# Kernel optimization log

Measured on AMD Instinct MI355X. Metric: run time of the kernel, lower is better.

Reference implementation:

```python
import jax, jax.numpy as jnp
import numpy as np

N_NODES = 16384
N_EDGES = 131072
EDGE_DIM = 16
IN_CH = 32
OUT_CH = 32
HID_EDGE = 64
MLP_HID = 64  # int(32 * 2.0)
OUT_FINAL = 10
N_GRAPHS = 64
BN_EPS = 1e-5


def setup_inputs() -> dict:
    key = jax.random.key(0)
    ks = jax.random.split(key, 20)
    s = lambda *sh: 1.0 / np.sqrt(sh[0])
    inp = {
        'x': jax.random.normal(ks[0], (N_NODES, IN_CH), jnp.float32),
        'edge_attr': jax.random.normal(ks[1], (N_EDGES, EDGE_DIM), jnp.float32),
        'edge_index': jax.random.randint(ks[2], (2, N_EDGES), 0, N_NODES, jnp.int64),
        'batch': jnp.sort(jax.random.randint(ks[3], (N_NODES,), 0, N_GRAPHS, jnp.int64)),
    }
    # layer 0: edge MLP (EDGE_DIM->HID_EDGE->IN_CH*OUT_CH), root, bias, BN affine
    inp['w1_0'] = jax.random.normal(ks[4], (EDGE_DIM, HID_EDGE), jnp.float32) * s(EDGE_DIM)
    inp['b1_0'] = jnp.zeros((HID_EDGE,), jnp.float32)
    inp['w2_0'] = jax.random.normal(ks[5], (HID_EDGE, IN_CH * OUT_CH), jnp.float32) * s(HID_EDGE)
    inp['b2_0'] = jnp.zeros((IN_CH * OUT_CH,), jnp.float32)
    inp['root_0'] = jax.random.normal(ks[6], (IN_CH, OUT_CH), jnp.float32) * s(IN_CH)
    inp['bias_0'] = jnp.zeros((OUT_CH,), jnp.float32)
    inp['gamma_0'] = jnp.ones((OUT_CH,), jnp.float32)
    inp['beta_0'] = jnp.zeros((OUT_CH,), jnp.float32)
    # layer 1: edge MLP (EDGE_DIM->HID_EDGE->OUT_CH*OUT_CH)
    inp['w1_1'] = jax.random.normal(ks[7], (EDGE_DIM, HID_EDGE), jnp.float32) * s(EDGE_DIM)
    inp['b1_1'] = jnp.zeros((HID_EDGE,), jnp.float32)
    inp['w2_1'] = jax.random.normal(ks[8], (HID_EDGE, OUT_CH * OUT_CH), jnp.float32) * s(HID_EDGE)
    inp['b2_1'] = jnp.zeros((OUT_CH * OUT_CH,), jnp.float32)
    inp['root_1'] = jax.random.normal(ks[9], (OUT_CH, OUT_CH), jnp.float32) * s(OUT_CH)
    inp['bias_1'] = jnp.zeros((OUT_CH,), jnp.float32)
    inp['gamma_1'] = jnp.ones((OUT_CH,), jnp.float32)
    inp['beta_1'] = jnp.zeros((OUT_CH,), jnp.float32)
    # final MLP (dropout is identity in eval / deterministic reference)
    inp['mlp_w1'] = jax.random.normal(ks[10], (OUT_CH, MLP_HID), jnp.float32) * s(OUT_CH)
    inp['mlp_b1'] = jnp.zeros((MLP_HID,), jnp.float32)
    inp['mlp_w2'] = jax.random.normal(ks[11], (MLP_HID, OUT_FINAL), jnp.float32) * s(MLP_HID)
    inp['mlp_b2'] = jnp.zeros((OUT_FINAL,), jnp.float32)
    return inp


def _nnconv(x, src, dst, edge_attr, w1, b1, w2, b2, root, bias, out_ch):
    # per-edge weight matrices from the edge MLP: [E, in, out]
    h = jax.nn.relu(edge_attr @ w1 + b1)
    W = (h @ w2 + b2).reshape(-1, x.shape[1], out_ch)
    msg = jnp.einsum('ei,eio->eo', x[src], W)  # gather + per-edge matmul
    agg = jax.ops.segment_sum(msg, dst, num_segments=N_NODES)
    cnt = jax.ops.segment_sum(jnp.ones((dst.shape[0], 1), x.dtype), dst, num_segments=N_NODES)
    agg = agg / jnp.maximum(cnt, 1.0)  # scatter-mean (zero-degree nodes -> 0)
    return agg + x @ root + bias


def _bn(x, gamma, beta):
    m = jnp.mean(x, axis=0)
    v = jnp.var(x, axis=0)
    return (x - m) * jax.lax.rsqrt(v + BN_EPS) * gamma + beta


def reference(x, edge_attr, edge_index, batch,
              w1_0, b1_0, w2_0, b2_0, root_0, bias_0, gamma_0, beta_0,
              w1_1, b1_1, w2_1, b2_1, root_1, bias_1, gamma_1, beta_1,
              mlp_w1, mlp_b1, mlp_w2, mlp_b2):
    src, dst = edge_index[0], edge_index[1]
    h = _nnconv(x, src, dst, edge_attr, w1_0, b1_0, w2_0, b2_0, root_0, bias_0, OUT_CH)
    h = jax.nn.relu(_bn(h, gamma_0, beta_0))
    h = _nnconv(h, src, dst, edge_attr, w1_1, b1_1, w2_1, b2_1, root_1, bias_1, OUT_CH)
    h = jax.nn.relu(_bn(h, gamma_1, beta_1))
    # global mean pool over graphs
    pooled = jax.ops.segment_sum(h, batch, num_segments=N_GRAPHS)
    gcnt = jax.ops.segment_sum(jnp.ones((h.shape[0], 1), h.dtype), batch, num_segments=N_GRAPHS)
    pooled = pooled / jnp.maximum(gcnt, 1.0)
    logits = jax.nn.relu(pooled @ mlp_w1 + mlp_b1) @ mlp_w2 + mlp_b2
    return logits
```

## Files before the change

kernel.cpp:

```cpp
#include <hip/hip_runtime.h>
#include <hip/hip_bf16.h>

#define NN 16384
#define NE 131072
#define NG 64
#define EPB 128

typedef unsigned short u16;
typedef unsigned int u32;
typedef __attribute__((ext_vector_type(8))) short short8;
typedef __attribute__((ext_vector_type(4))) float f32x4;
typedef __attribute__((ext_vector_type(2))) float f32x2;

__device__ __forceinline__ float bf2f(u16 u) {
    u32 x = ((u32)u) << 16;
    return __builtin_bit_cast(float, x);
}
__device__ __forceinline__ u16 f2bf(float f) {
    u32 u = __builtin_bit_cast(u32, f);
    u = u + 0x7fffu + ((u >> 16) & 1u);
    return (u16)(u >> 16);
}
__device__ __forceinline__ u32 pk2bf(float a, float b) {
    return (u32)f2bf(a) | ((u32)f2bf(b) << 16);
}
#if __has_builtin(__builtin_amdgcn_cvt_pk_bf16_f32)
__device__ __forceinline__ u32 pk2bf_fast(float a, float b) {
    auto v = __builtin_amdgcn_cvt_pk_bf16_f32(a, b);
    static_assert(sizeof(v) == 4, "cvt_pk_bf16 size");
    return __builtin_bit_cast(u32, v);
}
#else
__device__ __forceinline__ u32 pk2bf_fast(float a, float b) {
    u32 ua = __builtin_bit_cast(u32, a) + 0x8000u;
    u32 ub = __builtin_bit_cast(u32, b) + 0x8000u;
    return __builtin_amdgcn_perm(ub, ua, 0x07060302u);
}
#endif
__device__ __forceinline__ float toF(float f) { return f; }
__device__ __forceinline__ float toF(u16 u) { return bf2f(u); }

__device__ __forceinline__ float loadF(const void* p, int i, bool bf) {
    return bf ? bf2f(((const u16*)p)[i]) : ((const float*)p)[i];
}
__device__ __forceinline__ int loadI(const void* p, int i, bool i64) {
    return i64 ? (int)((const long long*)p)[i] : ((const int*)p)[i];
}
__device__ __forceinline__ bool det_bf(const void* g0) {
    return ((const u16*)g0)[0] == 0x3F80u;
}
__device__ __forceinline__ bool det_i64(const void* eidx) {
    const u32* u = (const u32*)eidx;
    return (u[1] | u[3] | u[5] | u[7]) == 0u;
}

__global__ __launch_bounds__(256) void k_prep(const void* w2a, const void* b2a,
                                              const void* w2b, const void* b2b,
                                              u16* bp0, u16* bp1, const void* g0) {
    const bool bf = det_bf(g0);
    int id = blockIdx.x * 256 + threadIdx.x;
    if (id >= 2 * 66560) return;
    int l = id / 66560, v = id % 66560;
    int j = v & 7, lane = (v >> 3) & 63, nt = (v >> 9) & 1, t = v >> 10;
    int kk = (lane >> 4) * 8 + j;
    int n = (lane & 15) + 16 * nt;
    const void* w2 = l ? w2b : w2a;
    const void* b2 = l ? b2b : b2a;
    float val = (t < 64) ? loadF(w2, t * 1024 + kk * 32 + n, bf)
                         : loadF(b2, kk * 32 + n, bf);
    (l ? bp1 : bp0)[v] = f2bf(val);
}

__global__ __launch_bounds__(256) void k_cnt(const void* eidx, float* cnt) {
    const bool i64 = det_i64(eidx);
    int e = blockIdx.x * 256 + threadIdx.x;
    int d = loadI(eidx, NE + e, i64);
    atomicAdd(&cnt[d], 1.0f);
}

template <typename T>
__device__ __forceinline__ void compute_h_half(const void* eav, const void* w1v, const void* b1v,
                                               int e, int kh, float* hv) {
    const T* w1 = (const T*)w1v;
    const T* b1 = (const T*)b1v;
    float ein[16];
    if (sizeof(T) == 2) {
        const uint4* er = (const uint4*)((const char*)eav + (size_t)e * 32);
        uint4 ra = er[0], rb = er[1];
        u32 wds[8] = {ra.x, ra.y, ra.z, ra.w, rb.x, rb.y, rb.z, rb.w};
#pragma unroll
        for (int k2 = 0; k2 < 8; k2++) {
            ein[2 * k2]     = bf2f((u16)(wds[k2] & 0xffffu));
            ein[2 * k2 + 1] = bf2f((u16)(wds[k2] >> 16));
        }
    } else {
        const float4* er = (const float4*)((const char*)eav + (size_t)e * 64);
        float4 r0 = er[0], r1 = er[1], r2 = er[2], r3 = er[3];
        ein[0] = r0.x; ein[1] = r0.y; ein[2] = r0.z; ein[3] = r0.w;
        ein[4] = r1.x; ein[5] = r1.y; ein[6] = r1.z; ein[7] = r1.w;
        ein[8] = r2.x; ein[9] = r2.y; ein[10] = r2.z; ein[11] = r2.w;
        ein[12] = r3.x; ein[13] = r3.y; ein[14] = r3.z; ein[15] = r3.w;
    }
    const int kb = kh * 32;
#pragma unroll
    for (int k = 0; k < 32; k++) hv[k] = toF(b1[kb + k]);
#pragma unroll 4
    for (int d = 0; d < 16; d++) {
        float ed = ein[d];
#pragma unroll
        for (int k = 0; k < 32; k++) hv[k] += ed * toF(w1[d * 64 + kb + k]);
    }
}

#define HSTR 72
__global__ __launch_bounds__(256, 4) void k_edge(const void* ea, const void* w1, const void* b1,
                                                 const void* xv, int x_f32,
                                                 const void* eidx, const u16* Bpack,
                                                 float* agg, const void* g0) {
    const bool bf = det_bf(g0);
    const bool i64 = det_i64(eidx);
    __shared__ __align__(16) u16 hl[EPB * HSTR];
    const int tid = threadIdx.x;
    const int e0 = blockIdx.x * EPB;

    {
        const int el = tid & (EPB - 1);
        const int kh = tid >> 7;
        float hv[32];
        if (bf) compute_h_half<u16>(ea, w1, b1, e0 + el, kh, hv);
        else    compute_h_half<float>(ea, w1, b1, e0 + el, kh, hv);
        u32* row = (u32*)&hl[el * HSTR] + kh * 16;
#pragma unroll
        for (int tt = 0; tt < 16; tt++)
            row[tt] = pk2bf_fast(fmaxf(hv[2 * tt], 0.f), fmaxf(hv[2 * tt + 1], 0.f));
    }
    __syncthreads();

    const int lane = tid & 63;
    const int w = tid >> 6;
    const int q = lane >> 4;
    const int m = lane & 15;
    const int wbl = w * 32;
    const int wb = e0 + wbl;
    const bool xf = (x_f32 != 0) || (!bf);
    f32x2 xr2[2][4];
#pragma unroll
    for (int mt = 0; mt < 2; mt++) {
        int s = loadI(eidx, wb + mt * 16 + m, i64);
        if (xf) {
            const float4* xp = (const float4*)xv + (size_t)s * 8 + q * 2;
            float4 a = xp[0], b = xp[1];
            xr2[mt][0] = f32x2{a.x, a.y}; xr2[mt][1] = f32x2{a.z, a.w};
            xr2[mt][2] = f32x2{b.x, b.y}; xr2[mt][3] = f32x2{b.z, b.w};
        } else {
            const uint4* xp = (const uint4*)((const char*)xv + (size_t)s * 64 + q * 16);
            uint4 a = *xp;
            xr2[mt][0] = f32x2{bf2f((u16)(a.x & 0xffff)), bf2f((u16)(a.x >> 16))};
            xr2[mt][1] = f32x2{bf2f((u16)(a.y & 0xffff)), bf2f((u16)(a.y >> 16))};
            xr2[mt][2] = f32x2{bf2f((u16)(a.z & 0xffff)), bf2f((u16)(a.z >> 16))};
            xr2[mt][3] = f32x2{bf2f((u16)(a.w & 0xffff)), bf2f((u16)(a.w >> 16))};
        }
    }

    f32x4 acc[2][2];
#pragma unroll
    for (int mt = 0; mt < 2; mt++) {
        acc[mt][0] = f32x4{0.f, 0.f, 0.f, 0.f};
        acc[mt][1] = f32x4{0.f, 0.f, 0.f, 0.f};
    }
    const uint4* bp = (const uint4*)Bpack;
    int rowb[2];
#pragma unroll
    for (int mt = 0; mt < 2; mt++) rowb[mt] = (wbl + mt * 16 + m) * HSTR;

    uint4 nb0 = bp[lane];
    uint4 nb1 = bp[64 + lane];
    for (int tc = 0; tc < 8; tc++) {
        uint4 hb[2];
#pragma unroll
        for (int mt = 0; mt < 2; mt++)
            hb[mt] = *(const uint4*)&hl[rowb[mt] + tc * 8];
#pragma unroll
        for (int tj = 0; tj < 8; tj++) {
            int t = tc * 8 + tj;
            uint4 bu0 = nb0, bu1 = nb1;
            nb0 = bp[((t + 1) * 2 + 0) * 64 + lane];
            nb1 = bp[((t + 1) * 2 + 1) * 64 + lane];
            short8 B0 = __builtin_bit_cast(short8, bu0);
            short8 B1 = __builtin_bit_cast(short8, bu1);
#pragma unroll
            for (int mt = 0; mt < 2; mt++) {
                u32 wd = ((const u32*)&hb[mt])[tj >> 1];
                u32 hbits = (tj & 1) ? (wd & 0xFFFF0000u) : (wd << 16);
                float hs = __builtin_bit_cast(float, hbits);
                f32x2 h2 = {hs, hs};
                f32x2 p0 = h2 * xr2[mt][0];
                f32x2 p1 = h2 * xr2[mt][1];
                f32x2 p2 = h2 * xr2[mt][2];
                f32x2 p3 = h2 * xr2[mt][3];
                uint4 au = make_uint4(pk2bf_fast(p0.x, p0.y), pk2bf_fast(p1.x, p1.y),
                                      pk2bf_fast(p2.x, p2.y), pk2bf_fast(p3.x, p3.y));
                short8 A = __builtin_bit_cast(short8, au);
                acc[mt][0] = __builtin_amdgcn_mfma_f32_16x16x32_bf16(A, B0, acc[mt][0], 0, 0, 0);
                acc[mt][1] = __builtin_amdgcn_mfma_f32_16x16x32_bf16(A, B1, acc[mt][1], 0, 0, 0);
            }
        }
    }
    {
        short8 B0 = __builtin_bit_cast(short8, nb0);
        short8 B1 = __builtin_bit_cast(short8, nb1);
#pragma unroll
        for (int mt = 0; mt < 2; mt++) {
            uint4 au = make_uint4(pk2bf_fast(xr2[mt][0].x, xr2[mt][0].y),
                                  pk2bf_fast(xr2[mt][1].x, xr2[mt][1].y),
                                  pk2bf_fast(xr2[mt][2].x, xr2[mt][2].y),
                                  pk2bf_fast(xr2[mt][3].x, xr2[mt][3].y));
            short8 A = __builtin_bit_cast(short8, au);
            acc[mt][0] = __builtin_amdgcn_mfma_f32_16x16x32_bf16(A, B0, acc[mt][0], 0, 0, 0);
            acc[mt][1] = __builtin_amdgcn_mfma_f32_16x16x32_bf16(A, B1, acc[mt][1], 0, 0, 0);
        }
    }

#pragma unroll
    for (int mt = 0; mt < 2; mt++) {
        int eb = wb + mt * 16 + q * 4;
#pragma unroll
        for (int r = 0; r < 4; r++) {
            int dst = loadI(eidx, NE + eb + r, i64);
            float* ap = agg + (size_t)dst * 32 + m;
            atomicAdd(ap, acc[mt][0][r]);
            atomicAdd(ap + 16, acc[mt][1][r]);
        }
    }
}

__global__ __launch_bounds__(256) void k_node(const float* agg, const float* cnt,
                                              const void* xv, int x_f32,
                                              const void* root, const void* bias,
                                              float* hpre, float* sS, float* sQ,
                                              const void* g0) {
    const bool bf = det_bf(g0);
    const int tid = threadIdx.x;
    const int v = blockIdx.x * 8 + (tid >> 5);
    const int o = tid & 31;
    const bool xf = (x_f32 != 0) || (!bf);
    float xrow[32];
    if (xf) {
        const float* x = (const float*)xv + (size_t)v * 32;
#pragma unroll
        for (int i = 0; i < 32; i++) xrow[i] = x[i];
    } else {
        const u16* x = (const u16*)xv + (size_t)v * 32;
#pragma unroll
        for (int i = 0; i < 32; i++) xrow[i] = bf2f(x[i]);
    }
    float a;
    if (bf) {
        const u16* R = (const u16*)root;
        a = bf2f(((const u16*)bias)[o]);
#pragma unroll
        for (int i = 0; i < 32; i++) a += xrow[i] * bf2f(R[i * 32 + o]);
    } else {
        const float* R = (const float*)root;
        a = ((const float*)bias)[o];
#pragma unroll
        for (int i = 0; i < 32; i++) a += xrow[i] * R[i * 32 + o];
    }
    float pre = agg[(size_t)v * 32 + o] / fmaxf(cnt[v], 1.0f) + a;
    hpre[(size_t)v * 32 + o] = pre;

    __shared__ float lS[256], lQ[256];
    lS[tid] = pre;
    lQ[tid] = pre * pre;
    __syncthreads();
#pragma unroll
    for (int off = 128; off >= 32; off >>= 1) {
        if (tid < off) { lS[tid] += lS[tid + off]; lQ[tid] += lQ[tid + off]; }
        __syncthreads();
    }
    if (tid < 32) {
        int slot = (blockIdx.x & 15) * 32 + tid;
        atomicAdd(&sS[slot], lS[tid]);
        atomicAdd(&sQ[slot], lQ[tid]);
    }
}

__global__ __launch_bounds__(256) void k_bn(const float* hpre, const float* sS, const float* sQ,
                                            const void* gamma, const void* beta, float* hout,
                                            const void* g0) {
    const bool bf = det_bf(g0);
    const int tid = threadIdx.x;
    const int v = blockIdx.x * 8 + (tid >> 5);
    const int o = tid & 31;
    float s = 0.f, qq = 0.f;
#pragma unroll
    for (int p = 0; p < 16; p++) { s += sS[p * 32 + o]; qq += sQ[p * 32 + o]; }
    float mn = s * (1.0f / 16384.0f);
    float var = qq * (1.0f / 16384.0f) - mn * mn;
    float inv = rsqrtf(var + 1e-5f);
    float g = loadF(gamma, o, bf), b = loadF(beta, o, bf);
    float y = (hpre[(size_t)v * 32 + o] - mn) * inv * g + b;
    hout[(size_t)v * 32 + o] = fmaxf(y, 0.f);
}

__global__ __launch_bounds__(256) void k_bnpool(const float* hpre, const float* sS, const float* sQ,
                                                const void* gamma, const void* beta,
                                                const void* batch, float* pooled, float* gcnt,
                                                const void* eidx, const void* g0) {
    const bool bf = det_bf(g0);
    const bool i64 = det_i64(eidx);
    const int tid = threadIdx.x;
    const int o = tid & 31;
    const int c = tid >> 5;
    float s = 0.f, qq = 0.f;
#pragma unroll
    for (int p = 0; p < 16; p++) { s += sS[p * 32 + o]; qq += sQ[p * 32 + o]; }
    float mn = s * (1.0f / 16384.0f);
    float var = qq * (1.0f / 16384.0f) - mn * mn;
    float inv = rsqrtf(var + 1e-5f);
    float gg = loadF(gamma, o, bf), bb = loadF(beta, o, bf);

    const int base = blockIdx.x * 256 + c;
    float acc = 0.f, cacc = 0.f;
    int curg = -1;
#pragma unroll 4
    for (int j = 0; j < 32; j++) {
        int v = base + j * 8;
        int g = loadI(batch, v, i64);
        float y = fmaxf((hpre[(size_t)v * 32 + o] - mn) * inv * gg + bb, 0.f);
        if (g != curg) {
            if (curg >= 0) {
                atomicAdd(&pooled[curg * 32 + o], acc);
                if (o == 0) atomicAdd(&gcnt[curg], cacc);
            }
            acc = 0.f; cacc = 0.f; curg = g;
        }
        acc += y; cacc += 1.f;
    }
    if (curg >= 0) {
        atomicAdd(&pooled[curg * 32 + o], acc);
        if (o == 0) atomicAdd(&gcnt[curg], cacc);
    }
}

__global__ __launch_bounds__(64) void k_final(const float* pooled, const float* gcnt,
                        const void* w1, const void* b1, const void* w2, const void* b2,
                        void* out, const void* g0) {
    const bool bf = det_bf(g0);
    const int g = blockIdx.x;
    const int j = threadIdx.x;
    float inv = 1.0f / fmaxf(gcnt[g], 1.0f);
    float a = loadF(b1, j, bf);
#pragma unroll
    for (int i = 0; i < 32; i++) {
        float p = pooled[g * 32 + i] * inv;
        a += p * loadF(w1, i * 64 + j, bf);
    }
    a = fmaxf(a, 0.f);
    float lg[10];
#pragma unroll
    for (int c = 0; c < 10; c++) lg[c] = a * loadF(w2, j * 10 + c, bf);
#pragma unroll
    for (int off = 32; off >= 1; off >>= 1) {
#pragma unroll
        for (int c = 0; c < 10; c++) lg[c] += __shfl_down(lg[c], off, 64);
    }
    if (j == 0) {
        if (bf) {
            u16* op = (u16*)out;
#pragma unroll
            for (int c = 0; c < 10; c++) op[g * 10 + c] = f2bf(lg[c] + loadF(b2, c, bf));
        } else {
            float* op = (float*)out;
#pragma unroll
            for (int c = 0; c < 10; c++) op[g * 10 + c] = lg[c] + loadF(b2, c, bf);
        }
    }
}

extern "C" void kernel_launch(void* const* d_in, const int* in_sizes, int n_in,
                              void* d_out, int out_size, void* d_ws, size_t ws_size,
                              hipStream_t stream) {
    char* ws = (char*)d_ws;
    u16* bp0 = (u16*)(ws + 256);
    u16* bp1 = (u16*)(ws + 256 + 133120);
    char* zbase = ws + 266496;
    float* agg    = (float*)(zbase);
    float* cnt    = (float*)(zbase + 2097152);
    float* sS0    = (float*)(zbase + 2162688);
    float* sQ0    = (float*)(zbase + 2164736);
    float* sS1    = (float*)(zbase + 2166784);
    float* sQ1    = (float*)(zbase + 2168832);
    float* pooled = (float*)(zbase + 2170880);
    float* gcnt   = (float*)(zbase + 2179072);
    const size_t zsize = 2179328;
    float* hpre = (float*)(ws + 266496 + 2179328);
    float* hout = (float*)(ws + 266496 + 2179328 + 2097152);

    const void* x     = d_in[0];
    const void* ea    = d_in[1];
    const void* eidx  = d_in[2];
    const void* batch = d_in[3];
    const void* g0    = d_in[10];

    (void)hipMemsetAsync(zbase, 0, zsize, stream);
    k_prep<<<520, 256, 0, stream>>>(d_in[6], d_in[7], d_in[14], d_in[15], bp0, bp1, g0);
    k_cnt<<<NE / 256, 256, 0, stream>>>(eidx, cnt);

    k_edge<<<NE / EPB, 256, 0, stream>>>(ea, d_in[4], d_in[5], x, 0, eidx, bp0, agg, g0);
    k_node<<<NN / 8, 256, 0, stream>>>(agg, cnt, x, 0, d_in[8], d_in[9], hpre, sS0, sQ0, g0);
    k_bn<<<NN / 8, 256, 0, stream>>>(hpre, sS0, sQ0, d_in[10], d_in[11], hout, g0);

    (void)hipMemsetAsync(agg, 0, 2097152, stream);

    k_edge<<<NE / EPB, 256, 0, stream>>>(ea, d_in[12], d_in[13], hout, 1, eidx, bp1, agg, g0);
    k_node<<<NN / 8, 256, 0, stream>>>(agg, cnt, hout, 1, d_in[16], d_in[17], hpre, sS1, sQ1, g0);

    k_bnpool<<<NN / 256, 256, 0, stream>>>(hpre, sS1, sQ1, d_in[18], d_in[19], batch,
                                           pooled, gcnt, eidx, g0);
    k_final<<<NG, 64, 0, stream>>>(pooled, gcnt, d_in[20], d_in[21], d_in[22], d_in[23], d_out, g0);
}
```

Before: 251.0 us.

## Compute edge-MLP hidden layer with MFMA and merge prep kernels

Replaces the scalar FMA computation of the first edge-MLP layer with bf16 MFMA instructions, using a new prepacked, zero-padded w1 layout built in the prep kernel. The edge-count kernel is folded into the prep kernel to drop one launch. The Bpack prefetch in the main MFMA loop becomes a 4-deep register ring instead of a single-step lookahead. This adds bf16 rounding of edge attributes and uses more registers, which may affect occupancy.

```diff
diff --git a/kernel.cpp b/kernel.cpp
--- a/kernel.cpp
+++ b/kernel.cpp
@@ -37,9 +37,6 @@
     return __builtin_amdgcn_perm(ub, ua, 0x07060302u);
 }
 #endif
-__device__ __forceinline__ float toF(float f) { return f; }
-__device__ __forceinline__ float toF(u16 u) { return bf2f(u); }
-
 __device__ __forceinline__ float loadF(const void* p, int i, bool bf) {
     return bf ? bf2f(((const u16*)p)[i]) : ((const float*)p)[i];
 }
@@ -56,64 +53,40 @@
 
 __global__ __launch_bounds__(256) void k_prep(const void* w2a, const void* b2a,
                                               const void* w2b, const void* b2b,
-                                              u16* bp0, u16* bp1, const void* g0) {
+                                              const void* w1a, const void* w1b,
+                                              u16* bp0, u16* bp1, u16* w1p0, u16* w1p1,
+                                              const void* eidx, float* cnt, const void* g0) {
     const bool bf = det_bf(g0);
     int id = blockIdx.x * 256 + threadIdx.x;
-    if (id >= 2 * 66560) return;
-    int l = id / 66560, v = id % 66560;
-    int j = v & 7, lane = (v >> 3) & 63, nt = (v >> 9) & 1, t = v >> 10;
-    int kk = (lane >> 4) * 8 + j;
-    int n = (lane & 15) + 16 * nt;
-    const void* w2 = l ? w2b : w2a;
-    const void* b2 = l ? b2b : b2a;
-    float val = (t < 64) ? loadF(w2, t * 1024 + kk * 32 + n, bf)
-                         : loadF(b2, kk * 32 + n, bf);
-    (l ? bp1 : bp0)[v] = f2bf(val);
-}
-
-__global__ __launch_bounds__(256) void k_cnt(const void* eidx, float* cnt) {
-    const bool i64 = det_i64(eidx);
-    int e = blockIdx.x * 256 + threadIdx.x;
-    int d = loadI(eidx, NE + e, i64);
-    atomicAdd(&cnt[d], 1.0f);
-}
-
-template <typename T>
-__device__ __forceinline__ void compute_h_half(const void* eav, const void* w1v, const void* b1v,
-                                               int e, int kh, float* hv) {
-    const T* w1 = (const T*)w1v;
-    const T* b1 = (const T*)b1v;
-    float ein[16];
-    if (sizeof(T) == 2) {
-        const uint4* er = (const uint4*)((const char*)eav + (size_t)e * 32);
-        uint4 ra = er[0], rb = er[1];
-        u32 wds[8] = {ra.x, ra.y, ra.z, ra.w, rb.x, rb.y, rb.z, rb.w};
-#pragma unroll
-        for (int k2 = 0; k2 < 8; k2++) {
-            ein[2 * k2]     = bf2f((u16)(wds[k2] & 0xffffu));
-            ein[2 * k2 + 1] = bf2f((u16)(wds[k2] >> 16));
-        }
+    if (id < 2 * 66560) {
+        int l = id / 66560, v = id % 66560;
+        int j = v & 7, lane = (v >> 3) & 63, nt = (v >> 9) & 1, t = v >> 10;
+        int kk = (lane >> 4) * 8 + j;
+        int n = (lane & 15) + 16 * nt;
+        const void* w2 = l ? w2b : w2a;
+        const void* b2 = l ? b2b : b2a;
+        float val = (t < 64) ? loadF(w2, t * 1024 + kk * 32 + n, bf)
+                             : loadF(b2, kk * 32 + n, bf);
+        (l ? bp1 : bp0)[v] = f2bf(val);
+    } else if (id < 2 * 66560 + 2 * 2048) {
+        int v = id - 2 * 66560;
+        int l = v >> 11; v &= 2047;
+        int j = v & 7, lane = (v >> 3) & 63, nt = v >> 9;
+        int k = (lane >> 4) * 8 + j;
+        int n = nt * 16 + (lane & 15);
+        const void* w1 = l ? w1b : w1a;
+        float val = (k < 16) ? loadF(w1, k * 64 + n, bf) : 0.f;
+        (l ? w1p1 : w1p0)[v] = f2bf(val);
     } else {
-        const float4* er = (const float4*)((const char*)eav + (size_t)e * 64);
-        float4 r0 = er[0], r1 = er[1], r2 = er[2], r3 = er[3];
-        ein[0] = r0.x; ein[1] = r0.y; ein[2] = r0.z; ein[3] = r0.w;
-        ein[4] = r1.x; ein[5] = r1.y; ein[6] = r1.z; ein[7] = r1.w;
-        ein[8] = r2.x; ein[9] = r2.y; ein[10] = r2.z; ein[11] = r2.w;
-        ein[12] = r3.x; ein[13] = r3.y; ein[14] = r3.z; ein[15] = r3.w;
-    }
-    const int kb = kh * 32;
-#pragma unroll
-    for (int k = 0; k < 32; k++) hv[k] = toF(b1[kb + k]);
-#pragma unroll 4
-    for (int d = 0; d < 16; d++) {
-        float ed = ein[d];
-#pragma unroll
-        for (int k = 0; k < 32; k++) hv[k] += ed * toF(w1[d * 64 + kb + k]);
+        const bool i64 = det_i64(eidx);
+        int e = id - (2 * 66560 + 2 * 2048);
+        int d = loadI(eidx, NE + e, i64);
+        atomicAdd(&cnt[d], 1.0f);
     }
 }
 
 #define HSTR 72
-__global__ __launch_bounds__(256, 4) void k_edge(const void* ea, const void* w1, const void* b1,
+__global__ __launch_bounds__(256, 4) void k_edge(const void* ea, const u16* w1p, const void* b1,
                                                  const void* xv, int x_f32,
                                                  const void* eidx, const u16* Bpack,
                                                  float* agg, const void* g0) {
@@ -122,26 +95,49 @@
     __shared__ __align__(16) u16 hl[EPB * HSTR];
     const int tid = threadIdx.x;
     const int e0 = blockIdx.x * EPB;
-
-    {
-        const int el = tid & (EPB - 1);
-        const int kh = tid >> 7;
-        float hv[32];
-        if (bf) compute_h_half<u16>(ea, w1, b1, e0 + el, kh, hv);
-        else    compute_h_half<float>(ea, w1, b1, e0 + el, kh, hv);
-        u32* row = (u32*)&hl[el * HSTR] + kh * 16;
-#pragma unroll
-        for (int tt = 0; tt < 16; tt++)
-            row[tt] = pk2bf_fast(fmaxf(hv[2 * tt], 0.f), fmaxf(hv[2 * tt + 1], 0.f));
-    }
-    __syncthreads();
-
     const int lane = tid & 63;
     const int w = tid >> 6;
     const int q = lane >> 4;
     const int m = lane & 15;
     const int wbl = w * 32;
     const int wb = e0 + wbl;
+
+    {
+        short8 Ah[2];
+#pragma unroll
+        for (int e2 = 0; e2 < 2; e2++) {
+            int eg = wb + e2 * 16 + m;
+            uint4 av = make_uint4(0u, 0u, 0u, 0u);
+            if (bf) {
+                uint4 t = *(const uint4*)((const char*)ea + (size_t)eg * 32 + (q & 1) * 16);
+                if (q < 2) av = t;
+            } else {
+                const float4* p = (const float4*)((const char*)ea + (size_t)eg * 64 + (q & 1) * 32);
+                float4 a = p[0], b = p[1];
+                if (q < 2) av = make_uint4(pk2bf_fast(a.x, a.y), pk2bf_fast(a.z, a.w),
+                                           pk2bf_fast(b.x, b.y), pk2bf_fast(b.z, b.w));
+            }
+            Ah[e2] = __builtin_bit_cast(short8, av);
+        }
+#pragma unroll
+        for (int nt = 0; nt < 4; nt++) {
+            uint4 bw = *(const uint4*)&w1p[(nt * 64 + lane) * 8];
+            short8 Bf = __builtin_bit_cast(short8, bw);
+            float bb = loadF(b1, nt * 16 + m, bf);
+#pragma unroll
+            for (int e2 = 0; e2 < 2; e2++) {
+                f32x4 c = __builtin_amdgcn_mfma_f32_16x16x32_bf16(
+                    Ah[e2], Bf, f32x4{0.f, 0.f, 0.f, 0.f}, 0, 0, 0);
+                int rbase = (wbl + e2 * 16 + q * 4) * HSTR + nt * 16 + m;
+#pragma unroll
+                for (int r = 0; r < 4; r++) {
+                    u32 pkd = pk2bf_fast(fmaxf(c[r] + bb, 0.f), 0.f);
+                    hl[rbase + r * HSTR] = (u16)pkd;
+                }
+            }
+        }
+    }
+
     const bool xf = (x_f32 != 0) || (!bf);
     f32x2 xr2[2][4];
 #pragma unroll
@@ -162,30 +158,38 @@
         }
     }
 
+    const uint4* bp4 = (const uint4*)Bpack;
+    uint4 pb[4][2];
+#pragma unroll
+    for (int d = 0; d < 4; d++) {
+        pb[d][0] = bp4[(d * 2 + 0) * 64 + lane];
+        pb[d][1] = bp4[(d * 2 + 1) * 64 + lane];
+    }
+
+    __syncthreads();
+
     f32x4 acc[2][2];
 #pragma unroll
     for (int mt = 0; mt < 2; mt++) {
         acc[mt][0] = f32x4{0.f, 0.f, 0.f, 0.f};
         acc[mt][1] = f32x4{0.f, 0.f, 0.f, 0.f};
     }
-    const uint4* bp = (const uint4*)Bpack;
     int rowb[2];
 #pragma unroll
     for (int mt = 0; mt < 2; mt++) rowb[mt] = (wbl + mt * 16 + m) * HSTR;
 
-    uint4 nb0 = bp[lane];
-    uint4 nb1 = bp[64 + lane];
     for (int tc = 0; tc < 8; tc++) {
         uint4 hb[2];
-#pragma unroll
-        for (int mt = 0; mt < 2; mt++)
-            hb[mt] = *(const uint4*)&hl[rowb[mt] + tc * 8];
+        hb[0] = *(const uint4*)&hl[rowb[0] + tc * 8];
+        hb[1] = *(const uint4*)&hl[rowb[1] + tc * 8];
 #pragma unroll
         for (int tj = 0; tj < 8; tj++) {
             int t = tc * 8 + tj;
-            uint4 bu0 = nb0, bu1 = nb1;
-            nb0 = bp[((t + 1) * 2 + 0) * 64 + lane];
-            nb1 = bp[((t + 1) * 2 + 1) * 64 + lane];
+            int slot = tj & 3;
+            uint4 bu0 = pb[slot][0], bu1 = pb[slot][1];
+            int tn = t + 4; if (tn > 64) tn = 64;
+            pb[slot][0] = bp4[(tn * 2 + 0) * 64 + lane];
+            pb[slot][1] = bp4[(tn * 2 + 1) * 64 + lane];
             short8 B0 = __builtin_bit_cast(short8, bu0);
             short8 B1 = __builtin_bit_cast(short8, bu1);
 #pragma unroll
@@ -207,8 +211,8 @@
         }
     }
     {
-        short8 B0 = __builtin_bit_cast(short8, nb0);
-        short8 B1 = __builtin_bit_cast(short8, nb1);
+        short8 B0 = __builtin_bit_cast(short8, pb[0][0]);
+        short8 B1 = __builtin_bit_cast(short8, pb[0][1]);
 #pragma unroll
         for (int mt = 0; mt < 2; mt++) {
             uint4 au = make_uint4(pk2bf_fast(xr2[mt][0].x, xr2[mt][0].y),
@@ -382,9 +386,11 @@
                               void* d_out, int out_size, void* d_ws, size_t ws_size,
                               hipStream_t stream) {
     char* ws = (char*)d_ws;
-    u16* bp0 = (u16*)(ws + 256);
-    u16* bp1 = (u16*)(ws + 256 + 133120);
-    char* zbase = ws + 266496;
+    u16* bp0  = (u16*)(ws + 256);
+    u16* bp1  = (u16*)(ws + 256 + 133120);
+    u16* w1p0 = (u16*)(ws + 266496);
+    u16* w1p1 = (u16*)(ws + 270592);
+    char* zbase = ws + 274688;
     float* agg    = (float*)(zbase);
     float* cnt    = (float*)(zbase + 2097152);
     float* sS0    = (float*)(zbase + 2162688);
@@ -394,8 +400,8 @@
     float* pooled = (float*)(zbase + 2170880);
     float* gcnt   = (float*)(zbase + 2179072);
     const size_t zsize = 2179328;
-    float* hpre = (float*)(ws + 266496 + 2179328);
-    float* hout = (float*)(ws + 266496 + 2179328 + 2097152);
+    float* hpre = (float*)(ws + 274688 + 2179328);
+    float* hout = (float*)(ws + 274688 + 2179328 + 2097152);
 
     const void* x     = d_in[0];
     const void* ea    = d_in[1];
@@ -404,16 +410,17 @@
     const void* g0    = d_in[10];
 
     (void)hipMemsetAsync(zbase, 0, zsize, stream);
-    k_prep<<<520, 256, 0, stream>>>(d_in[6], d_in[7], d_in[14], d_in[15], bp0, bp1, g0);
-    k_cnt<<<NE / 256, 256, 0, stream>>>(eidx, cnt);
-
-    k_edge<<<NE / EPB, 256, 0, stream>>>(ea, d_in[4], d_in[5], x, 0, eidx, bp0, agg, g0);
+    k_prep<<<1048, 256, 0, stream>>>(d_in[6], d_in[7], d_in[14], d_in[15],
+                                     d_in[4], d_in[12],
+                                     bp0, bp1, w1p0, w1p1, eidx, cnt, g0);
+
+    k_edge<<<NE / EPB, 256, 0, stream>>>(ea, w1p0, d_in[5], x, 0, eidx, bp0, agg, g0);
     k_node<<<NN / 8, 256, 0, stream>>>(agg, cnt, x, 0, d_in[8], d_in[9], hpre, sS0, sQ0, g0);
     k_bn<<<NN / 8, 256, 0, stream>>>(hpre, sS0, sQ0, d_in[10], d_in[11], hout, g0);
 
     (void)hipMemsetAsync(agg, 0, 2097152, stream);
 
-    k_edge<<<NE / EPB, 256, 0, stream>>>(ea, d_in[12], d_in[13], hout, 1, eidx, bp1, agg, g0);
+    k_edge<<<NE / EPB, 256, 0, stream>>>(ea, w1p1, d_in[13], hout, 1, eidx, bp1, agg, g0);
     k_node<<<NN / 8, 256, 0, stream>>>(agg, cnt, hout, 1, d_in[16], d_in[17], hpre, sS1, sQ1, g0);
 
     k_bnpool<<<NN / 256, 256, 0, stream>>>(hpre, sS1, sQ1, d_in[18], d_in[19], batch,
```

Result: faster. 223.1 us (-11.1%).
